# Kernel optimization log

Measured on AMD Instinct MI355X. Metric: run time of the kernel, lower is better.

The kernel has to match this reference:

```python
import jax, jax.numpy as jnp
import numpy as np

N_NODES = 50000
N_EDGES = 800000
NFEAT, NHID1, NHID2, NHID3, NCLASS = 128, 128, 128, 64, 32


def _glorot(key, fan_in, fan_out):
    lim = 1.0 / np.sqrt(fan_in)
    return jax.random.uniform(key, (fan_in, fan_out), jnp.float32, -lim, lim)


def setup_inputs() -> dict:
    key = jax.random.key(0)
    ks = jax.random.split(key, 12)
    x = jax.random.normal(ks[0], (N_NODES, NFEAT), jnp.float32)
    edge_src = jax.random.randint(ks[1], (N_EDGES,), 0, N_NODES, jnp.int32)
    edge_dst = jax.random.randint(ks[2], (N_EDGES,), 0, N_NODES, jnp.int32)
    edge_val = jax.random.uniform(ks[3], (N_EDGES,), jnp.float32)
    W1 = _glorot(ks[4], NFEAT, NHID1)
    W2 = _glorot(ks[5], NHID1, NHID2)
    W3 = _glorot(ks[6], NHID2, NHID3)
    W4 = _glorot(ks[7], NHID3, NCLASS)
    b1 = jnp.zeros((NHID1,), jnp.float32)
    b2 = jnp.zeros((NHID2,), jnp.float32)
    b3 = jnp.zeros((NHID3,), jnp.float32)
    b4 = jnp.zeros((NCLASS,), jnp.float32)
    return {"x": x, "edge_src": edge_src, "edge_dst": edge_dst, "edge_val": edge_val,
            "W1": W1, "b1": b1, "W2": W2, "b2": b2, "W3": W3, "b3": b3, "W4": W4, "b4": b4}


def _gc_layer(h, W, b, src, dst, val):
    # support = h @ W ; out = adj @ support + b  (adj in COO form)
    support = h @ W                                   # [N, d_out]
    msgs = support[src] * val[:, None]                # [E, d_out] irregular gather
    agg = jax.ops.segment_sum(msgs, dst, num_segments=N_NODES)  # scatter-add
    return agg + b


def reference(x, edge_src, edge_dst, edge_val, W1, b1, W2, b2, W3, b3, W4, b4):
    h = jax.nn.relu(_gc_layer(x, W1, b1, edge_src, edge_dst, edge_val))
    h = jax.nn.relu(_gc_layer(h, W2, b2, edge_src, edge_dst, edge_val))
    h = jax.nn.relu(_gc_layer(h, W3, b3, edge_src, edge_dst, edge_val))
    h = _gc_layer(h, W4, b4, edge_src, edge_dst, edge_val)
    return h
```

## Files before the change

kernel.cpp:

```cpp
#include <hip/hip_runtime.h>

constexpr int NNODES = 50000;
constexpr int NEDGES = 800000;
constexpr int CAP = 64;

constexpr int NPART = 8;
constexpr int PSIZE = NNODES / NPART;
constexpr int FCH = 1024;
constexpr int QCAP = 320;

constexpr int CHUNKS = (NEDGES + FCH - 1) / FCH;
constexpr int TILE_ITEMS = (NNODES + 63) / 64;
constexpr int PACK_TOT = 43008;

typedef __attribute__((ext_vector_type(8))) short short8;
typedef __attribute__((ext_vector_type(8))) unsigned short ushort8;
typedef __attribute__((ext_vector_type(4))) float f32x4;

__device__ __forceinline__ unsigned short f2b(float f) {
    unsigned int u = __float_as_uint(f);
    u += 0x7FFFu + ((u >> 16) & 1u);
    return (unsigned short)(u >> 16);
}
__device__ __forceinline__ float b2f(unsigned short u) {
    return __uint_as_float(((unsigned int)u) << 16);
}
__device__ __forceinline__ float recval(unsigned int rec) {
    return __uint_as_float(rec & 0xFFFF0000u);
}

template <int N, int K>
__device__ __forceinline__ void pack_one(int idx, const float* __restrict__ W,
                                         unsigned short* __restrict__ Wp) {
    constexpr int KS = K / 32;
    int j = idx & 7;
    int lane = (idx >> 3) & 63;
    int t = idx >> 9;
    int nt = t / KS, ks = t % KS;
    int n = nt * 16 + (lane & 15);
    int k = ks * 32 + (lane >> 4) * 8 + j;
    Wp[idx] = f2b(W[(size_t)k * N + n]);
}

__global__ __launch_bounds__(256) void prep_kernel(
        const float* __restrict__ W1, const float* __restrict__ W2,
        const float* __restrict__ W3, const float* __restrict__ W4,
        unsigned short* __restrict__ Wp1, unsigned short* __restrict__ Wp2,
        unsigned short* __restrict__ Wp3, unsigned short* __restrict__ Wp4) {
    int p = blockIdx.x * 256 + threadIdx.x;
    if (p < 16384) pack_one<128, 128>(p, W1, Wp1);
    else if (p < 32768) pack_one<128, 128>(p - 16384, W2, Wp2);
    else if (p < 40960) pack_one<64, 128>(p - 32768, W3, Wp3);
    else if (p < 43008) pack_one<32, 64>(p - 40960, W4, Wp4);
}

template <int N, int K, bool AF32>
__device__ __forceinline__ void gemm_item(int t, const void* __restrict__ Hv,
                                          const unsigned short* __restrict__ Wp,
                                          unsigned short* __restrict__ Sb) {
    constexpr int NT = N / 16, KS = K / 32;
    const int lane = threadIdx.x & 63;
    const int wave = threadIdx.x >> 6;
    const int waveRow = t * 64 + wave * 16;
    const int m = lane & 15, quad = lane >> 4;
    int arow = waveRow + m;
    if (arow >= NNODES) arow = NNODES - 1;

    f32x4 acc[NT];
#pragma unroll
    for (int nt = 0; nt < NT; ++nt) acc[nt] = (f32x4){0.f, 0.f, 0.f, 0.f};

#pragma unroll
    for (int ks = 0; ks < KS; ++ks) {
        short8 a;
        if (AF32) {
            const float* hp = (const float*)Hv + (size_t)arow * K + ks * 32 + quad * 8;
            float4 a0 = *reinterpret_cast<const float4*>(hp);
            float4 a1 = *reinterpret_cast<const float4*>(hp + 4);
            a[0] = (short)f2b(a0.x); a[1] = (short)f2b(a0.y);
            a[2] = (short)f2b(a0.z); a[3] = (short)f2b(a0.w);
            a[4] = (short)f2b(a1.x); a[5] = (short)f2b(a1.y);
            a[6] = (short)f2b(a1.z); a[7] = (short)f2b(a1.w);
        } else {
            a = *reinterpret_cast<const short8*>(
                (const unsigned short*)Hv + (size_t)arow * K + ks * 32 + quad * 8);
        }
#pragma unroll
        for (int nt = 0; nt < NT; ++nt) {
            short8 b = *reinterpret_cast<const short8*>(Wp + ((nt * KS + ks) * 64 + lane) * 8);
            acc[nt] = __builtin_amdgcn_mfma_f32_16x16x32_bf16(a, b, acc[nt], 0, 0, 0);
        }
    }

#pragma unroll
    for (int reg = 0; reg < 4; ++reg) {
        int grow = waveRow + quad * 4 + reg;
        if (grow < NNODES) {
#pragma unroll
            for (int nt = 0; nt < NT; ++nt)
                Sb[(size_t)grow * N + nt * 16 + m] = f2b(acc[nt][reg]);
        }
    }
}

__global__ __launch_bounds__(256) void fill_gemm1_kernel(
        const int* __restrict__ src, const int* __restrict__ dst,
        const float* __restrict__ val, int* __restrict__ cursor,
        unsigned int* __restrict__ buckets,
        const float* __restrict__ x, const unsigned short* __restrict__ Wp1,
        unsigned short* __restrict__ Q) {
    __shared__ unsigned int q_rec[QCAP];
    __shared__ int q_d[QCAP];
    __shared__ int qcount;

    const int g = blockIdx.x / 9;
    const int r = blockIdx.x % 9;
    if (r == 0) {
        gemm_item<128, 128, true>(g, x, Wp1, Q);
        return;
    }

    if (threadIdx.x == 0) qcount = 0;
    __syncthreads();

    const int part = blockIdx.x & 7;
    const int lo = part * PSIZE, hi = lo + PSIZE;
    const int e0 = g * FCH + threadIdx.x * 4;

    int4 d4 = make_int4(-1, -1, -1, -1);
    int4 s4 = make_int4(0, 0, 0, 0);
    float4 v4 = make_float4(0.f, 0.f, 0.f, 0.f);
    if (e0 + 3 < NEDGES) {
        d4 = *reinterpret_cast<const int4*>(dst + e0);
        s4 = *reinterpret_cast<const int4*>(src + e0);
        v4 = *reinterpret_cast<const float4*>(val + e0);
    } else if (e0 < NEDGES) {
        d4.x = dst[e0]; s4.x = src[e0]; v4.x = val[e0];
        if (e0 + 1 < NEDGES) { d4.y = dst[e0 + 1]; s4.y = src[e0 + 1]; v4.y = val[e0 + 1]; }
        if (e0 + 2 < NEDGES) { d4.z = dst[e0 + 2]; s4.z = src[e0 + 2]; v4.z = val[e0 + 2]; }
    }
    int dd[4] = {d4.x, d4.y, d4.z, d4.w};
    int ss[4] = {s4.x, s4.y, s4.z, s4.w};
    float vv[4] = {v4.x, v4.y, v4.z, v4.w};
#pragma unroll
    for (int i = 0; i < 4; ++i) {
        int d = dd[i];
        if (d >= lo && d < hi) {
            unsigned int rec = (unsigned int)ss[i] | ((unsigned int)f2b(vv[i]) << 16);
            int pos = atomicAdd(&qcount, 1);
            if (pos < QCAP) {
                q_rec[pos] = rec;
                q_d[pos] = d;
            } else {
                int p = atomicAdd(&cursor[d], 1);
                if (p < CAP) buckets[(size_t)d * CAP + p] = rec;
            }
        }
    }
    __syncthreads();

    int n = qcount < QCAP ? qcount : QCAP;
    for (int i = threadIdx.x; i < n; i += 256) {
        int d = q_d[i];
        unsigned int rec = q_rec[i];
        int p = atomicAdd(&cursor[d], 1);
        if (p < CAP) buckets[(size_t)d * CAP + p] = rec;
    }
}

template <int NIN, int NOUT>
__global__ __launch_bounds__(256) void agg_gemm_kernel(
        const unsigned short* __restrict__ Sprev, const unsigned int* __restrict__ buckets,
        const int* __restrict__ counts, const float* __restrict__ bias,
        const unsigned short* __restrict__ Wp, unsigned short* __restrict__ Snext) {
    constexpr int NCH = NIN / 8;
    constexpr int R = 256 / NCH;
    constexpr int LROW = NIN + 8;
    constexpr int KS = NIN / 32;
    constexpr int NT = NOUT / 16;
    constexpr int RT = R / 16;
    constexpr int TILES = RT * NT;
    __shared__ unsigned short htile[R * LROW];

    const int nodeBase = blockIdx.x * R;

    {
        int nl = threadIdx.x / NCH;
        int cg = threadIdx.x % NCH;
        int node = nodeBase + nl;
        float acc[8];
        if (node < NNODES) {
#pragma unroll
            for (int t = 0; t < 8; ++t) acc[t] = bias[cg * 8 + t];
            int cnt = counts[node];
            if (cnt > CAP) cnt = CAP;
            const unsigned int* eb = buckets + (size_t)node * CAP;
            int j = 0;
            for (; j + 4 <= cnt; j += 4) {
                uint4 ea = *reinterpret_cast<const uint4*>(eb + j);
                const ushort8 m0 = *reinterpret_cast<const ushort8*>(Sprev + (size_t)(ea.x & 0xFFFF) * NIN + cg * 8);
                const ushort8 m1 = *reinterpret_cast<const ushort8*>(Sprev + (size_t)(ea.y & 0xFFFF) * NIN + cg * 8);
                const ushort8 m2 = *reinterpret_cast<const ushort8*>(Sprev + (size_t)(ea.z & 0xFFFF) * NIN + cg * 8);
                const ushort8 m3 = *reinterpret_cast<const ushort8*>(Sprev + (size_t)(ea.w & 0xFFFF) * NIN + cg * 8);
                float v0 = recval(ea.x), v1 = recval(ea.y);
                float v2 = recval(ea.z), v3 = recval(ea.w);
#pragma unroll
                for (int t = 0; t < 8; ++t) {
                    acc[t] = fmaf(b2f(m0[t]), v0, acc[t]);
                    acc[t] = fmaf(b2f(m1[t]), v1, acc[t]);
                    acc[t] = fmaf(b2f(m2[t]), v2, acc[t]);
                    acc[t] = fmaf(b2f(m3[t]), v3, acc[t]);
                }
            }
            for (; j < cnt; ++j) {
                unsigned int rec = eb[j];
                float v = recval(rec);
                const ushort8 mr = *reinterpret_cast<const ushort8*>(Sprev + (size_t)(rec & 0xFFFF) * NIN + cg * 8);
#pragma unroll
                for (int t = 0; t < 8; ++t) acc[t] = fmaf(b2f(mr[t]), v, acc[t]);
            }
        } else {
#pragma unroll
            for (int t = 0; t < 8; ++t) acc[t] = 0.f;
        }
        ushort8 o;
#pragma unroll
        for (int t = 0; t < 8; ++t) o[t] = f2b(fmaxf(acc[t], 0.f));
        *reinterpret_cast<ushort8*>(&htile[nl * LROW + cg * 8]) = o;
    }
    __syncthreads();

    {
        const int lane = threadIdx.x & 63, wave = threadIdx.x >> 6;
        const int m = lane & 15, quad = lane >> 4;
        for (int t = wave; t < TILES; t += 4) {
            int rt = t / NT, nt = t % NT;
            f32x4 acc = (f32x4){0.f, 0.f, 0.f, 0.f};
#pragma unroll
            for (int ks = 0; ks < KS; ++ks) {
                short8 a = *reinterpret_cast<const short8*>(
                    &htile[(rt * 16 + m) * LROW + ks * 32 + quad * 8]);
                short8 b = *reinterpret_cast<const short8*>(Wp + ((nt * KS + ks) * 64 + lane) * 8);
                acc = __builtin_amdgcn_mfma_f32_16x16x32_bf16(a, b, acc, 0, 0, 0);
            }
#pragma unroll
            for (int reg = 0; reg < 4; ++reg) {
                int grow = nodeBase + rt * 16 + quad * 4 + reg;
                if (grow < NNODES)
                    Snext[(size_t)grow * NOUT + nt * 16 + m] = f2b(acc[reg]);
            }
        }
    }
}

__global__ __launch_bounds__(256) void agg_out_kernel(const unsigned short* __restrict__ Sb,
        const unsigned int* __restrict__ buckets, const int* __restrict__ counts,
        const float* __restrict__ bias, float* __restrict__ outp) {
    constexpr int N = 32;
    int node = blockIdx.x * 64 + threadIdx.x / 4;
    int cg = threadIdx.x % 4;
    if (node >= NNODES) return;
    int cnt = counts[node];
    if (cnt > CAP) cnt = CAP;
    const unsigned int* eb = buckets + (size_t)node * CAP;
    float acc[8];
#pragma unroll
    for (int t = 0; t < 8; ++t) acc[t] = bias[cg * 8 + t];

    int j = 0;
    for (; j + 4 <= cnt; j += 4) {
        uint4 ea = *reinterpret_cast<const uint4*>(eb + j);
        const ushort8 m0 = *reinterpret_cast<const ushort8*>(Sb + (size_t)(ea.x & 0xFFFF) * N + cg * 8);
        const ushort8 m1 = *reinterpret_cast<const ushort8*>(Sb + (size_t)(ea.y & 0xFFFF) * N + cg * 8);
        const ushort8 m2 = *reinterpret_cast<const ushort8*>(Sb + (size_t)(ea.z & 0xFFFF) * N + cg * 8);
        const ushort8 m3 = *reinterpret_cast<const ushort8*>(Sb + (size_t)(ea.w & 0xFFFF) * N + cg * 8);
        float v0 = recval(ea.x), v1 = recval(ea.y);
        float v2 = recval(ea.z), v3 = recval(ea.w);
#pragma unroll
        for (int t = 0; t < 8; ++t) {
            acc[t] = fmaf(b2f(m0[t]), v0, acc[t]);
            acc[t] = fmaf(b2f(m1[t]), v1, acc[t]);
            acc[t] = fmaf(b2f(m2[t]), v2, acc[t]);
            acc[t] = fmaf(b2f(m3[t]), v3, acc[t]);
        }
    }
    for (; j < cnt; ++j) {
        unsigned int rec = eb[j];
        float v = recval(rec);
        const ushort8 mr = *reinterpret_cast<const ushort8*>(Sb + (size_t)(rec & 0xFFFF) * N + cg * 8);
#pragma unroll
        for (int t = 0; t < 8; ++t) acc[t] = fmaf(b2f(mr[t]), v, acc[t]);
    }

    float* op = outp + (size_t)node * N + cg * 8;
    *reinterpret_cast<float4*>(op) = make_float4(acc[0], acc[1], acc[2], acc[3]);
    *reinterpret_cast<float4*>(op + 4) = make_float4(acc[4], acc[5], acc[6], acc[7]);
}

extern "C" void kernel_launch(void* const* d_in, const int* in_sizes, int n_in,
                              void* d_out, int out_size, void* d_ws, size_t ws_size,
                              hipStream_t stream) {
    const float* x   = (const float*)d_in[0];
    const int*   src = (const int*)d_in[1];
    const int*   dst = (const int*)d_in[2];
    const float* val = (const float*)d_in[3];
    const float* W1  = (const float*)d_in[4];
    const float* b1  = (const float*)d_in[5];
    const float* W2  = (const float*)d_in[6];
    const float* b2  = (const float*)d_in[7];
    const float* W3  = (const float*)d_in[8];
    const float* b3  = (const float*)d_in[9];
    const float* W4  = (const float*)d_in[10];
    const float* b4  = (const float*)d_in[11];
    float* out = (float*)d_out;

    unsigned short* P = (unsigned short*)d_ws;
    unsigned short* Q = P + (size_t)NNODES * 128;
    unsigned int* buckets = (unsigned int*)(Q + (size_t)NNODES * 128);
    unsigned short* Wp1 = (unsigned short*)(buckets + (size_t)NNODES * CAP);
    unsigned short* Wp2 = Wp1 + 128 * 128;
    unsigned short* Wp3 = Wp2 + 128 * 128;
    unsigned short* Wp4 = Wp3 + 128 * 64;
    int* cursor = (int*)(Wp4 + 64 * 32);

    const dim3 blk(256);

    hipMemsetAsync(cursor, 0, NNODES * sizeof(int), stream);
    prep_kernel<<<(PACK_TOT + 255) / 256, blk, 0, stream>>>(W1, W2, W3, W4,
                                                            Wp1, Wp2, Wp3, Wp4);
    fill_gemm1_kernel<<<CHUNKS * 9, blk, 0, stream>>>(
        src, dst, val, cursor, buckets, x, Wp1, Q);
    agg_gemm_kernel<128, 128><<<(NNODES + 15) / 16, blk, 0, stream>>>(
        Q, buckets, cursor, b1, Wp2, P);
    agg_gemm_kernel<128, 64><<<(NNODES + 15) / 16, blk, 0, stream>>>(
        P, buckets, cursor, b2, Wp3, Q);
    agg_gemm_kernel<64, 32><<<(NNODES + 31) / 32, blk, 0, stream>>>(
        Q, buckets, cursor, b3, Wp4, P);
    agg_out_kernel<<<(NNODES + 63) / 64, blk, 0, stream>>>(P, buckets, cursor, b4, out);
}
```

Measured before the change: 220.6 us.

## Replace fixed-capacity edge buckets with compact CSR built by histogram and scan

The fixed 64-slot per-node bucket array is replaced by a compact CSR layout. A degree histogram is fused with the first GEMM, followed by a two-pass prefix scan (rows padded to multiples of 4) and a scatter pass that writes edge records into contiguous rows. This shrinks the edge storage footprint and makes aggregation reads contiguous. It also removes the CAP truncation, so high-degree nodes are no longer silently dropped. The aggregation loop is unrolled to 8 edges to keep more gathers in flight, at the cost of two extra scan launches and a separate histogram pass over dst.

```diff
diff --git a/kernel.cpp b/kernel.cpp
--- a/kernel.cpp
+++ b/kernel.cpp
@@ -2,15 +2,16 @@
 
 constexpr int NNODES = 50000;
 constexpr int NEDGES = 800000;
-constexpr int CAP = 64;
 
 constexpr int NPART = 8;
 constexpr int PSIZE = NNODES / NPART;
 constexpr int FCH = 1024;
 constexpr int QCAP = 320;
-
 constexpr int CHUNKS = (NEDGES + FCH - 1) / FCH;
 constexpr int TILE_ITEMS = (NNODES + 63) / 64;
+constexpr int HCH = 512;
+constexpr int SCAN_BLOCKS = (NNODES + 255) / 256;
+constexpr int RECCAP = NEDGES + 3 * NNODES + 272;
 constexpr int PACK_TOT = 43008;
 
 typedef __attribute__((ext_vector_type(8))) short short8;
@@ -103,29 +104,81 @@
     }
 }
 
-__global__ __launch_bounds__(256) void fill_gemm1_kernel(
+__global__ __launch_bounds__(256) void gemm1_hist_kernel(
+        const float* __restrict__ x, const unsigned short* __restrict__ Wp1,
+        unsigned short* __restrict__ Q,
+        const int* __restrict__ dst, int* __restrict__ deg) {
+    const int g = blockIdx.x / 3;
+    const int r = blockIdx.x % 3;
+    if (r == 0) {
+        gemm_item<128, 128, true>(g, x, Wp1, Q);
+        return;
+    }
+    const int c = g * 2 + (r - 1);
+    const int e0 = c * HCH + threadIdx.x * 2;
+    if (e0 + 1 < NEDGES) {
+        int2 d2 = *reinterpret_cast<const int2*>(dst + e0);
+        atomicAdd(&deg[d2.x], 1);
+        atomicAdd(&deg[d2.y], 1);
+    } else if (e0 < NEDGES) {
+        atomicAdd(&deg[dst[e0]], 1);
+    }
+}
+
+__global__ __launch_bounds__(256) void scan1_kernel(const int* __restrict__ deg,
+        int* __restrict__ rowstart, int* __restrict__ blockSums) {
+    __shared__ int s[256];
+    const int b = blockIdx.x, tid = threadIdx.x;
+    const int i = b * 256 + tid;
+    int c = 0;
+    if (i < NNODES) c = (deg[i] + 3) & ~3;
+    s[tid] = c;
+    __syncthreads();
+    for (int o = 1; o < 256; o <<= 1) {
+        int t = (tid >= o) ? s[tid - o] : 0;
+        __syncthreads();
+        s[tid] += t;
+        __syncthreads();
+    }
+    if (i < NNODES) rowstart[i] = s[tid] - c;
+    if (tid == 255) blockSums[b] = s[255];
+}
+
+__global__ __launch_bounds__(256) void scan2_kernel(const int* __restrict__ blockSums,
+        int* __restrict__ rowstart, int* __restrict__ cursor) {
+    __shared__ int s[256];
+    const int b = blockIdx.x, tid = threadIdx.x;
+    s[tid] = (tid < SCAN_BLOCKS) ? blockSums[tid] : 0;
+    __syncthreads();
+    for (int o = 1; o < 256; o <<= 1) {
+        int t = (tid >= o) ? s[tid - o] : 0;
+        __syncthreads();
+        s[tid] += t;
+        __syncthreads();
+    }
+    const int off = (b == 0) ? 0 : s[b - 1];
+    const int i = b * 256 + tid;
+    if (i < NNODES) {
+        int rs = rowstart[i] + off;
+        rowstart[i] = rs;
+        cursor[i] = rs;
+    }
+}
+
+__global__ __launch_bounds__(256) void scatter_kernel(
         const int* __restrict__ src, const int* __restrict__ dst,
         const float* __restrict__ val, int* __restrict__ cursor,
-        unsigned int* __restrict__ buckets,
-        const float* __restrict__ x, const unsigned short* __restrict__ Wp1,
-        unsigned short* __restrict__ Q) {
+        unsigned int* __restrict__ rec) {
     __shared__ unsigned int q_rec[QCAP];
     __shared__ int q_d[QCAP];
     __shared__ int qcount;
-
-    const int g = blockIdx.x / 9;
-    const int r = blockIdx.x % 9;
-    if (r == 0) {
-        gemm_item<128, 128, true>(g, x, Wp1, Q);
-        return;
-    }
-
     if (threadIdx.x == 0) qcount = 0;
     __syncthreads();
 
     const int part = blockIdx.x & 7;
+    const int chunk = blockIdx.x >> 3;
     const int lo = part * PSIZE, hi = lo + PSIZE;
-    const int e0 = g * FCH + threadIdx.x * 4;
+    const int e0 = chunk * FCH + threadIdx.x * 4;
 
     int4 d4 = make_int4(-1, -1, -1, -1);
     int4 s4 = make_int4(0, 0, 0, 0);
@@ -146,14 +199,14 @@
     for (int i = 0; i < 4; ++i) {
         int d = dd[i];
         if (d >= lo && d < hi) {
-            unsigned int rec = (unsigned int)ss[i] | ((unsigned int)f2b(vv[i]) << 16);
+            unsigned int r = (unsigned int)ss[i] | ((unsigned int)f2b(vv[i]) << 16);
             int pos = atomicAdd(&qcount, 1);
             if (pos < QCAP) {
-                q_rec[pos] = rec;
+                q_rec[pos] = r;
                 q_d[pos] = d;
             } else {
                 int p = atomicAdd(&cursor[d], 1);
-                if (p < CAP) buckets[(size_t)d * CAP + p] = rec;
+                rec[p] = r;
             }
         }
     }
@@ -162,16 +215,72 @@
     int n = qcount < QCAP ? qcount : QCAP;
     for (int i = threadIdx.x; i < n; i += 256) {
         int d = q_d[i];
-        unsigned int rec = q_rec[i];
         int p = atomicAdd(&cursor[d], 1);
-        if (p < CAP) buckets[(size_t)d * CAP + p] = rec;
+        rec[p] = q_rec[i];
+    }
+}
+
+template <int NIN>
+__device__ __forceinline__ void pull_agg(const unsigned short* __restrict__ Sprev,
+                                         const unsigned int* __restrict__ eb,
+                                         int cnt, int cg, float* __restrict__ acc) {
+    const unsigned short* Sp = Sprev + cg * 8;
+    int j = 0;
+    for (; j + 8 <= cnt; j += 8) {
+        uint4 ea = *reinterpret_cast<const uint4*>(eb + j);
+        uint4 ec = *reinterpret_cast<const uint4*>(eb + j + 4);
+        const ushort8 m0 = *reinterpret_cast<const ushort8*>(Sp + (ea.x & 0xFFFFu) * (unsigned)NIN);
+        const ushort8 m1 = *reinterpret_cast<const ushort8*>(Sp + (ea.y & 0xFFFFu) * (unsigned)NIN);
+        const ushort8 m2 = *reinterpret_cast<const ushort8*>(Sp + (ea.z & 0xFFFFu) * (unsigned)NIN);
+        const ushort8 m3 = *reinterpret_cast<const ushort8*>(Sp + (ea.w & 0xFFFFu) * (unsigned)NIN);
+        const ushort8 m4 = *reinterpret_cast<const ushort8*>(Sp + (ec.x & 0xFFFFu) * (unsigned)NIN);
+        const ushort8 m5 = *reinterpret_cast<const ushort8*>(Sp + (ec.y & 0xFFFFu) * (unsigned)NIN);
+        const ushort8 m6 = *reinterpret_cast<const ushort8*>(Sp + (ec.z & 0xFFFFu) * (unsigned)NIN);
+        const ushort8 m7 = *reinterpret_cast<const ushort8*>(Sp + (ec.w & 0xFFFFu) * (unsigned)NIN);
+        float v0 = recval(ea.x), v1 = recval(ea.y), v2 = recval(ea.z), v3 = recval(ea.w);
+        float v4 = recval(ec.x), v5 = recval(ec.y), v6 = recval(ec.z), v7 = recval(ec.w);
+#pragma unroll
+        for (int t = 0; t < 8; ++t) {
+            acc[t] = fmaf(b2f(m0[t]), v0, acc[t]);
+            acc[t] = fmaf(b2f(m1[t]), v1, acc[t]);
+            acc[t] = fmaf(b2f(m2[t]), v2, acc[t]);
+            acc[t] = fmaf(b2f(m3[t]), v3, acc[t]);
+            acc[t] = fmaf(b2f(m4[t]), v4, acc[t]);
+            acc[t] = fmaf(b2f(m5[t]), v5, acc[t]);
+            acc[t] = fmaf(b2f(m6[t]), v6, acc[t]);
+            acc[t] = fmaf(b2f(m7[t]), v7, acc[t]);
+        }
+    }
+    for (; j + 4 <= cnt; j += 4) {
+        uint4 ea = *reinterpret_cast<const uint4*>(eb + j);
+        const ushort8 m0 = *reinterpret_cast<const ushort8*>(Sp + (ea.x & 0xFFFFu) * (unsigned)NIN);
+        const ushort8 m1 = *reinterpret_cast<const ushort8*>(Sp + (ea.y & 0xFFFFu) * (unsigned)NIN);
+        const ushort8 m2 = *reinterpret_cast<const ushort8*>(Sp + (ea.z & 0xFFFFu) * (unsigned)NIN);
+        const ushort8 m3 = *reinterpret_cast<const ushort8*>(Sp + (ea.w & 0xFFFFu) * (unsigned)NIN);
+        float v0 = recval(ea.x), v1 = recval(ea.y);
+        float v2 = recval(ea.z), v3 = recval(ea.w);
+#pragma unroll
+        for (int t = 0; t < 8; ++t) {
+            acc[t] = fmaf(b2f(m0[t]), v0, acc[t]);
+            acc[t] = fmaf(b2f(m1[t]), v1, acc[t]);
+            acc[t] = fmaf(b2f(m2[t]), v2, acc[t]);
+            acc[t] = fmaf(b2f(m3[t]), v3, acc[t]);
+        }
+    }
+    for (; j < cnt; ++j) {
+        unsigned int r = eb[j];
+        float v = recval(r);
+        const ushort8 mr = *reinterpret_cast<const ushort8*>(Sp + (r & 0xFFFFu) * (unsigned)NIN);
+#pragma unroll
+        for (int t = 0; t < 8; ++t) acc[t] = fmaf(b2f(mr[t]), v, acc[t]);
     }
 }
 
 template <int NIN, int NOUT>
 __global__ __launch_bounds__(256) void agg_gemm_kernel(
-        const unsigned short* __restrict__ Sprev, const unsigned int* __restrict__ buckets,
-        const int* __restrict__ counts, const float* __restrict__ bias,
+        const unsigned short* __restrict__ Sprev, const unsigned int* __restrict__ rec,
+        const int* __restrict__ rowstart, const int* __restrict__ rowend,
+        const float* __restrict__ bias,
         const unsigned short* __restrict__ Wp, unsigned short* __restrict__ Snext) {
     constexpr int NCH = NIN / 8;
     constexpr int R = 256 / NCH;
@@ -192,33 +301,9 @@
         if (node < NNODES) {
 #pragma unroll
             for (int t = 0; t < 8; ++t) acc[t] = bias[cg * 8 + t];
-            int cnt = counts[node];
-            if (cnt > CAP) cnt = CAP;
-            const unsigned int* eb = buckets + (size_t)node * CAP;
-            int j = 0;
-            for (; j + 4 <= cnt; j += 4) {
-                uint4 ea = *reinterpret_cast<const uint4*>(eb + j);
-                const ushort8 m0 = *reinterpret_cast<const ushort8*>(Sprev + (size_t)(ea.x & 0xFFFF) * NIN + cg * 8);
-                const ushort8 m1 = *reinterpret_cast<const ushort8*>(Sprev + (size_t)(ea.y & 0xFFFF) * NIN + cg * 8);
-                const ushort8 m2 = *reinterpret_cast<const ushort8*>(Sprev + (size_t)(ea.z & 0xFFFF) * NIN + cg * 8);
-                const ushort8 m3 = *reinterpret_cast<const ushort8*>(Sprev + (size_t)(ea.w & 0xFFFF) * NIN + cg * 8);
-                float v0 = recval(ea.x), v1 = recval(ea.y);
-                float v2 = recval(ea.z), v3 = recval(ea.w);
-#pragma unroll
-                for (int t = 0; t < 8; ++t) {
-                    acc[t] = fmaf(b2f(m0[t]), v0, acc[t]);
-                    acc[t] = fmaf(b2f(m1[t]), v1, acc[t]);
-                    acc[t] = fmaf(b2f(m2[t]), v2, acc[t]);
-                    acc[t] = fmaf(b2f(m3[t]), v3, acc[t]);
-                }
-            }
-            for (; j < cnt; ++j) {
-                unsigned int rec = eb[j];
-                float v = recval(rec);
-                const ushort8 mr = *reinterpret_cast<const ushort8*>(Sprev + (size_t)(rec & 0xFFFF) * NIN + cg * 8);
-#pragma unroll
-                for (int t = 0; t < 8; ++t) acc[t] = fmaf(b2f(mr[t]), v, acc[t]);
-            }
+            int start = rowstart[node];
+            int cnt = rowend[node] - start;
+            pull_agg<NIN>(Sprev, rec + start, cnt, cg, acc);
         } else {
 #pragma unroll
             for (int t = 0; t < 8; ++t) acc[t] = 0.f;
@@ -254,43 +339,20 @@
 }
 
 __global__ __launch_bounds__(256) void agg_out_kernel(const unsigned short* __restrict__ Sb,
-        const unsigned int* __restrict__ buckets, const int* __restrict__ counts,
-        const float* __restrict__ bias, float* __restrict__ outp) {
+        const unsigned int* __restrict__ rec, const int* __restrict__ rowstart,
+        const int* __restrict__ rowend, const float* __restrict__ bias,
+        float* __restrict__ outp) {
     constexpr int N = 32;
     int node = blockIdx.x * 64 + threadIdx.x / 4;
     int cg = threadIdx.x % 4;
     if (node >= NNODES) return;
-    int cnt = counts[node];
-    if (cnt > CAP) cnt = CAP;
-    const unsigned int* eb = buckets + (size_t)node * CAP;
     float acc[8];
 #pragma unroll
     for (int t = 0; t < 8; ++t) acc[t] = bias[cg * 8 + t];
 
-    int j = 0;
-    for (; j + 4 <= cnt; j += 4) {
-        uint4 ea = *reinterpret_cast<const uint4*>(eb + j);
-        const ushort8 m0 = *reinterpret_cast<const ushort8*>(Sb + (size_t)(ea.x & 0xFFFF) * N + cg * 8);
-        const ushort8 m1 = *reinterpret_cast<const ushort8*>(Sb + (size_t)(ea.y & 0xFFFF) * N + cg * 8);
-        const ushort8 m2 = *reinterpret_cast<const ushort8*>(Sb + (size_t)(ea.z & 0xFFFF) * N + cg * 8);
-        const ushort8 m3 = *reinterpret_cast<const ushort8*>(Sb + (size_t)(ea.w & 0xFFFF) * N + cg * 8);
-        float v0 = recval(ea.x), v1 = recval(ea.y);
-        float v2 = recval(ea.z), v3 = recval(ea.w);
-#pragma unroll
-        for (int t = 0; t < 8; ++t) {
-            acc[t] = fmaf(b2f(m0[t]), v0, acc[t]);
-            acc[t] = fmaf(b2f(m1[t]), v1, acc[t]);
-            acc[t] = fmaf(b2f(m2[t]), v2, acc[t]);
-            acc[t] = fmaf(b2f(m3[t]), v3, acc[t]);
-        }
-    }
-    for (; j < cnt; ++j) {
-        unsigned int rec = eb[j];
-        float v = recval(rec);
-        const ushort8 mr = *reinterpret_cast<const ushort8*>(Sb + (size_t)(rec & 0xFFFF) * N + cg * 8);
-#pragma unroll
-        for (int t = 0; t < 8; ++t) acc[t] = fmaf(b2f(mr[t]), v, acc[t]);
-    }
+    int start = rowstart[node];
+    int cnt = rowend[node] - start;
+    pull_agg<N>(Sb, rec + start, cnt, cg, acc);
 
     float* op = outp + (size_t)node * N + cg * 8;
     *reinterpret_cast<float4*>(op) = make_float4(acc[0], acc[1], acc[2], acc[3]);
@@ -316,25 +378,30 @@
 
     unsigned short* P = (unsigned short*)d_ws;
     unsigned short* Q = P + (size_t)NNODES * 128;
-    unsigned int* buckets = (unsigned int*)(Q + (size_t)NNODES * 128);
-    unsigned short* Wp1 = (unsigned short*)(buckets + (size_t)NNODES * CAP);
+    unsigned int* rec = (unsigned int*)(Q + (size_t)NNODES * 128);
+    int* deg       = (int*)(rec + RECCAP);
+    int* rowstart  = deg + NNODES;
+    int* cursor    = rowstart + NNODES;
+    int* blockSums = cursor + NNODES;
+    unsigned short* Wp1 = (unsigned short*)(blockSums + 256);
     unsigned short* Wp2 = Wp1 + 128 * 128;
     unsigned short* Wp3 = Wp2 + 128 * 128;
     unsigned short* Wp4 = Wp3 + 128 * 64;
-    int* cursor = (int*)(Wp4 + 64 * 32);
 
     const dim3 blk(256);
 
-    hipMemsetAsync(cursor, 0, NNODES * sizeof(int), stream);
+    hipMemsetAsync(deg, 0, NNODES * sizeof(int), stream);
     prep_kernel<<<(PACK_TOT + 255) / 256, blk, 0, stream>>>(W1, W2, W3, W4,
                                                             Wp1, Wp2, Wp3, Wp4);
-    fill_gemm1_kernel<<<CHUNKS * 9, blk, 0, stream>>>(
-        src, dst, val, cursor, buckets, x, Wp1, Q);
+    gemm1_hist_kernel<<<TILE_ITEMS * 3, blk, 0, stream>>>(x, Wp1, Q, dst, deg);
+    scan1_kernel<<<SCAN_BLOCKS, blk, 0, stream>>>(deg, rowstart, blockSums);
+    scan2_kernel<<<SCAN_BLOCKS, blk, 0, stream>>>(blockSums, rowstart, cursor);
+    scatter_kernel<<<CHUNKS * 8, blk, 0, stream>>>(src, dst, val, cursor, rec);
     agg_gemm_kernel<128, 128><<<(NNODES + 15) / 16, blk, 0, stream>>>(
-        Q, buckets, cursor, b1, Wp2, P);
+        Q, rec, rowstart, cursor, b1, Wp2, P);
     agg_gemm_kernel<128, 64><<<(NNODES + 15) / 16, blk, 0, stream>>>(
-        P, buckets, cursor, b2, Wp3, Q);
+        P, rec, rowstart, cursor, b2, Wp3, Q);
     agg_gemm_kernel<64, 32><<<(NNODES + 31) / 32, blk, 0, stream>>>(
-        Q, buckets, cursor, b3, Wp4, P);
-    agg_out_kernel<<<(NNODES + 63) / 64, blk, 0, stream>>>(P, buckets, cursor, b4, out);
-}
+        Q, rec, rowstart, cursor, b3, Wp4, P);
+    agg_out_kernel<<<(NNODES + 63) / 64, blk, 0, stream>>>(P, rec, rowstart, cursor, b4, out);
+}
```

New measurement: 261.3 us. 18.5% more time.

## Replace 8-pass edge bucketing with single-pass partition plus scatter kernel

Applied to the files above, without the earlier changes.

Previously the fill kernel ran 8 blocks per edge chunk, each rereading the chunk and keeping only edges whose destination fell in one node partition. Now each edge chunk is read once: edges are staged in shared memory per partition, flushed as 64-bit (dst, record) entries into per-partition global segments, and a separate scatter kernel then does the per-node cursor atomics into buckets. The cursor memset is folded into the weight-pack kernel, and the shared gather-accumulate loop is unrolled to 8 edges. This trades the redundant edge reads for an extra kernel launch and an extra write and read of an 8-byte-per-edge intermediate buffer. The scatter grid interleaves partitions across consecutive blocks, which may weaken the cache locality of the cursor atomics.

```diff
diff --git a/kernel.cpp b/kernel.cpp
--- a/kernel.cpp
+++ b/kernel.cpp
@@ -7,10 +7,11 @@
 constexpr int NPART = 8;
 constexpr int PSIZE = NNODES / NPART;
 constexpr int FCH = 1024;
-constexpr int QCAP = 320;
-
 constexpr int CHUNKS = (NEDGES + FCH - 1) / FCH;
 constexpr int TILE_ITEMS = (NNODES + 63) / 64;
+constexpr int LCAP = 192;
+constexpr int SEGSTRIDE = 131072;
+constexpr int SCHUNKS = SEGSTRIDE / FCH;
 constexpr int PACK_TOT = 43008;
 
 typedef __attribute__((ext_vector_type(8))) short short8;
@@ -46,8 +47,11 @@
         const float* __restrict__ W1, const float* __restrict__ W2,
         const float* __restrict__ W3, const float* __restrict__ W4,
         unsigned short* __restrict__ Wp1, unsigned short* __restrict__ Wp2,
-        unsigned short* __restrict__ Wp3, unsigned short* __restrict__ Wp4) {
+        unsigned short* __restrict__ Wp3, unsigned short* __restrict__ Wp4,
+        int* __restrict__ cursor, int* __restrict__ pcur) {
     int p = blockIdx.x * 256 + threadIdx.x;
+    if (p < NNODES) cursor[p] = 0;
+    if (p < 8) pcur[p] = 0;
     if (p < 16384) pack_one<128, 128>(p, W1, Wp1);
     else if (p < 32768) pack_one<128, 128>(p - 16384, W2, Wp2);
     else if (p < 40960) pack_one<64, 128>(p - 32768, W3, Wp3);
@@ -103,31 +107,27 @@
     }
 }
 
-__global__ __launch_bounds__(256) void fill_gemm1_kernel(
+__global__ __launch_bounds__(256) void gemm1_part_kernel(
+        const float* __restrict__ x, const unsigned short* __restrict__ Wp1,
+        unsigned short* __restrict__ Q,
         const int* __restrict__ src, const int* __restrict__ dst,
-        const float* __restrict__ val, int* __restrict__ cursor,
-        unsigned int* __restrict__ buckets,
-        const float* __restrict__ x, const unsigned short* __restrict__ Wp1,
-        unsigned short* __restrict__ Q) {
-    __shared__ unsigned int q_rec[QCAP];
-    __shared__ int q_d[QCAP];
-    __shared__ int qcount;
-
-    const int g = blockIdx.x / 9;
-    const int r = blockIdx.x % 9;
-    if (r == 0) {
+        const float* __restrict__ val,
+        int* __restrict__ pcur, unsigned long long* __restrict__ seg) {
+    __shared__ unsigned long long ls[8][LCAP];
+    __shared__ int lcnt[8];
+    __shared__ int gbase[8];
+
+    const int g = blockIdx.x >> 1;
+    if (blockIdx.x & 1) {
         gemm_item<128, 128, true>(g, x, Wp1, Q);
         return;
     }
 
-    if (threadIdx.x == 0) qcount = 0;
+    if (threadIdx.x < 8) lcnt[threadIdx.x] = 0;
     __syncthreads();
 
-    const int part = blockIdx.x & 7;
-    const int lo = part * PSIZE, hi = lo + PSIZE;
     const int e0 = g * FCH + threadIdx.x * 4;
-
-    int4 d4 = make_int4(-1, -1, -1, -1);
+    int4 d4 = make_int4(0, 0, 0, 0);
     int4 s4 = make_int4(0, 0, 0, 0);
     float4 v4 = make_float4(0.f, 0.f, 0.f, 0.f);
     if (e0 + 3 < NEDGES) {
@@ -144,27 +144,128 @@
     float vv[4] = {v4.x, v4.y, v4.z, v4.w};
 #pragma unroll
     for (int i = 0; i < 4; ++i) {
-        int d = dd[i];
-        if (d >= lo && d < hi) {
-            unsigned int rec = (unsigned int)ss[i] | ((unsigned int)f2b(vv[i]) << 16);
-            int pos = atomicAdd(&qcount, 1);
-            if (pos < QCAP) {
-                q_rec[pos] = rec;
-                q_d[pos] = d;
-            } else {
-                int p = atomicAdd(&cursor[d], 1);
-                if (p < CAP) buckets[(size_t)d * CAP + p] = rec;
+        if (e0 + i < NEDGES) {
+            int d = dd[i];
+            int part = d / PSIZE;
+            unsigned long long r = (unsigned long long)(unsigned)d |
+                ((unsigned long long)((unsigned)ss[i] | ((unsigned)f2b(vv[i]) << 16)) << 32);
+            int pos = atomicAdd(&lcnt[part], 1);
+            if (pos < LCAP) ls[part][pos] = r;
+            else {
+                int p = atomicAdd(&pcur[part], 1);
+                if (p < SEGSTRIDE) seg[(size_t)part * SEGSTRIDE + p] = r;
             }
         }
     }
     __syncthreads();
 
-    int n = qcount < QCAP ? qcount : QCAP;
-    for (int i = threadIdx.x; i < n; i += 256) {
-        int d = q_d[i];
-        unsigned int rec = q_rec[i];
-        int p = atomicAdd(&cursor[d], 1);
-        if (p < CAP) buckets[(size_t)d * CAP + p] = rec;
+    if (threadIdx.x < 8) {
+        int c = lcnt[threadIdx.x]; if (c > LCAP) c = LCAP;
+        gbase[threadIdx.x] = atomicAdd(&pcur[threadIdx.x], c);
+    }
+    __syncthreads();
+
+    int pre[9]; pre[0] = 0;
+#pragma unroll
+    for (int t = 0; t < 8; ++t) {
+        int c = lcnt[t]; if (c > LCAP) c = LCAP;
+        pre[t + 1] = pre[t] + c;
+    }
+    const int total = pre[8];
+    for (int i = threadIdx.x; i < total; i += 256) {
+        int part = 0;
+#pragma unroll
+        for (int t = 1; t < 8; ++t) part += (i >= pre[t]);
+        int off = i - pre[part];
+        int p = gbase[part] + off;
+        if (p < SEGSTRIDE) seg[(size_t)part * SEGSTRIDE + p] = ls[part][off];
+    }
+}
+
+__global__ __launch_bounds__(256) void scatter_kernel(
+        const unsigned long long* __restrict__ seg, const int* __restrict__ pcur,
+        int* __restrict__ cursor, unsigned int* __restrict__ buckets) {
+    const int part = blockIdx.x & 7;
+    const int chunk = blockIdx.x >> 3;
+    int cnt = pcur[part]; if (cnt > SEGSTRIDE) cnt = SEGSTRIDE;
+    const int r0 = chunk * FCH + threadIdx.x * 4;
+    if (r0 >= cnt) return;
+    const unsigned long long* sp = seg + (size_t)part * SEGSTRIDE;
+    if (r0 + 3 < cnt) {
+        uint4 a = *reinterpret_cast<const uint4*>(sp + r0);
+        uint4 b = *reinterpret_cast<const uint4*>(sp + r0 + 2);
+        int p0 = atomicAdd(&cursor[(int)a.x], 1);
+        if (p0 < CAP) buckets[(size_t)(int)a.x * CAP + p0] = a.y;
+        int p1 = atomicAdd(&cursor[(int)a.z], 1);
+        if (p1 < CAP) buckets[(size_t)(int)a.z * CAP + p1] = a.w;
+        int p2 = atomicAdd(&cursor[(int)b.x], 1);
+        if (p2 < CAP) buckets[(size_t)(int)b.x * CAP + p2] = b.y;
+        int p3 = atomicAdd(&cursor[(int)b.z], 1);
+        if (p3 < CAP) buckets[(size_t)(int)b.z * CAP + p3] = b.w;
+    } else {
+        for (int i = 0; i < cnt - r0; ++i) {
+            unsigned long long r = sp[r0 + i];
+            int d = (int)(unsigned)(r & 0xFFFFFFFFull);
+            unsigned int rc = (unsigned int)(r >> 32);
+            int p = atomicAdd(&cursor[d], 1);
+            if (p < CAP) buckets[(size_t)d * CAP + p] = rc;
+        }
+    }
+}
+
+template <int NIN>
+__device__ __forceinline__ void pull_agg(const unsigned short* __restrict__ Sprev,
+                                         const unsigned int* __restrict__ eb,
+                                         int cnt, int cg, float* __restrict__ acc) {
+    const unsigned short* Sp = Sprev + cg * 8;
+    int j = 0;
+    for (; j + 8 <= cnt; j += 8) {
+        uint4 ea = *reinterpret_cast<const uint4*>(eb + j);
+        uint4 ec = *reinterpret_cast<const uint4*>(eb + j + 4);
+        const ushort8 m0 = *reinterpret_cast<const ushort8*>(Sp + (ea.x & 0xFFFFu) * (unsigned)NIN);
+        const ushort8 m1 = *reinterpret_cast<const ushort8*>(Sp + (ea.y & 0xFFFFu) * (unsigned)NIN);
+        const ushort8 m2 = *reinterpret_cast<const ushort8*>(Sp + (ea.z & 0xFFFFu) * (unsigned)NIN);
+        const ushort8 m3 = *reinterpret_cast<const ushort8*>(Sp + (ea.w & 0xFFFFu) * (unsigned)NIN);
+        const ushort8 m4 = *reinterpret_cast<const ushort8*>(Sp + (ec.x & 0xFFFFu) * (unsigned)NIN);
+        const ushort8 m5 = *reinterpret_cast<const ushort8*>(Sp + (ec.y & 0xFFFFu) * (unsigned)NIN);
+        const ushort8 m6 = *reinterpret_cast<const ushort8*>(Sp + (ec.z & 0xFFFFu) * (unsigned)NIN);
+        const ushort8 m7 = *reinterpret_cast<const ushort8*>(Sp + (ec.w & 0xFFFFu) * (unsigned)NIN);
+        float v0 = recval(ea.x), v1 = recval(ea.y), v2 = recval(ea.z), v3 = recval(ea.w);
+        float v4 = recval(ec.x), v5 = recval(ec.y), v6 = recval(ec.z), v7 = recval(ec.w);
+#pragma unroll
+        for (int t = 0; t < 8; ++t) {
+            acc[t] = fmaf(b2f(m0[t]), v0, acc[t]);
+            acc[t] = fmaf(b2f(m1[t]), v1, acc[t]);
+            acc[t] = fmaf(b2f(m2[t]), v2, acc[t]);
+            acc[t] = fmaf(b2f(m3[t]), v3, acc[t]);
+            acc[t] = fmaf(b2f(m4[t]), v4, acc[t]);
+            acc[t] = fmaf(b2f(m5[t]), v5, acc[t]);
+            acc[t] = fmaf(b2f(m6[t]), v6, acc[t]);
+            acc[t] = fmaf(b2f(m7[t]), v7, acc[t]);
+        }
+    }
+    for (; j + 4 <= cnt; j += 4) {
+        uint4 ea = *reinterpret_cast<const uint4*>(eb + j);
+        const ushort8 m0 = *reinterpret_cast<const ushort8*>(Sp + (ea.x & 0xFFFFu) * (unsigned)NIN);
+        const ushort8 m1 = *reinterpret_cast<const ushort8*>(Sp + (ea.y & 0xFFFFu) * (unsigned)NIN);
+        const ushort8 m2 = *reinterpret_cast<const ushort8*>(Sp + (ea.z & 0xFFFFu) * (unsigned)NIN);
+        const ushort8 m3 = *reinterpret_cast<const ushort8*>(Sp + (ea.w & 0xFFFFu) * (unsigned)NIN);
+        float v0 = recval(ea.x), v1 = recval(ea.y);
+        float v2 = recval(ea.z), v3 = recval(ea.w);
+#pragma unroll
+        for (int t = 0; t < 8; ++t) {
+            acc[t] = fmaf(b2f(m0[t]), v0, acc[t]);
+            acc[t] = fmaf(b2f(m1[t]), v1, acc[t]);
+            acc[t] = fmaf(b2f(m2[t]), v2, acc[t]);
+            acc[t] = fmaf(b2f(m3[t]), v3, acc[t]);
+        }
+    }
+    for (; j < cnt; ++j) {
+        unsigned int r = eb[j];
+        float v = recval(r);
+        const ushort8 mr = *reinterpret_cast<const ushort8*>(Sp + (r & 0xFFFFu) * (unsigned)NIN);
+#pragma unroll
+        for (int t = 0; t < 8; ++t) acc[t] = fmaf(b2f(mr[t]), v, acc[t]);
     }
 }
 
@@ -194,31 +295,7 @@
             for (int t = 0; t < 8; ++t) acc[t] = bias[cg * 8 + t];
             int cnt = counts[node];
             if (cnt > CAP) cnt = CAP;
-            const unsigned int* eb = buckets + (size_t)node * CAP;
-            int j = 0;
-            for (; j + 4 <= cnt; j += 4) {
-                uint4 ea = *reinterpret_cast<const uint4*>(eb + j);
-                const ushort8 m0 = *reinterpret_cast<const ushort8*>(Sprev + (size_t)(ea.x & 0xFFFF) * NIN + cg * 8);
-                const ushort8 m1 = *reinterpret_cast<const ushort8*>(Sprev + (size_t)(ea.y & 0xFFFF) * NIN + cg * 8);
-                const ushort8 m2 = *reinterpret_cast<const ushort8*>(Sprev + (size_t)(ea.z & 0xFFFF) * NIN + cg * 8);
-                const ushort8 m3 = *reinterpret_cast<const ushort8*>(Sprev + (size_t)(ea.w & 0xFFFF) * NIN + cg * 8);
-                float v0 = recval(ea.x), v1 = recval(ea.y);
-                float v2 = recval(ea.z), v3 = recval(ea.w);
-#pragma unroll
-                for (int t = 0; t < 8; ++t) {
-                    acc[t] = fmaf(b2f(m0[t]), v0, acc[t]);
-                    acc[t] = fmaf(b2f(m1[t]), v1, acc[t]);
-                    acc[t] = fmaf(b2f(m2[t]), v2, acc[t]);
-                    acc[t] = fmaf(b2f(m3[t]), v3, acc[t]);
-                }
-            }
-            for (; j < cnt; ++j) {
-                unsigned int rec = eb[j];
-                float v = recval(rec);
-                const ushort8 mr = *reinterpret_cast<const ushort8*>(Sprev + (size_t)(rec & 0xFFFF) * NIN + cg * 8);
-#pragma unroll
-                for (int t = 0; t < 8; ++t) acc[t] = fmaf(b2f(mr[t]), v, acc[t]);
-            }
+            pull_agg<NIN>(Sprev, buckets + (size_t)node * CAP, cnt, cg, acc);
         } else {
 #pragma unroll
             for (int t = 0; t < 8; ++t) acc[t] = 0.f;
@@ -260,37 +337,13 @@
     int node = blockIdx.x * 64 + threadIdx.x / 4;
     int cg = threadIdx.x % 4;
     if (node >= NNODES) return;
+    float acc[8];
+#pragma unroll
+    for (int t = 0; t < 8; ++t) acc[t] = bias[cg * 8 + t];
+
     int cnt = counts[node];
     if (cnt > CAP) cnt = CAP;
-    const unsigned int* eb = buckets + (size_t)node * CAP;
-    float acc[8];
-#pragma unroll
-    for (int t = 0; t < 8; ++t) acc[t] = bias[cg * 8 + t];
-
-    int j = 0;
-    for (; j + 4 <= cnt; j += 4) {
-        uint4 ea = *reinterpret_cast<const uint4*>(eb + j);
-        const ushort8 m0 = *reinterpret_cast<const ushort8*>(Sb + (size_t)(ea.x & 0xFFFF) * N + cg * 8);
-        const ushort8 m1 = *reinterpret_cast<const ushort8*>(Sb + (size_t)(ea.y & 0xFFFF) * N + cg * 8);
-        const ushort8 m2 = *reinterpret_cast<const ushort8*>(Sb + (size_t)(ea.z & 0xFFFF) * N + cg * 8);
-        const ushort8 m3 = *reinterpret_cast<const ushort8*>(Sb + (size_t)(ea.w & 0xFFFF) * N + cg * 8);
-        float v0 = recval(ea.x), v1 = recval(ea.y);
-        float v2 = recval(ea.z), v3 = recval(ea.w);
-#pragma unroll
-        for (int t = 0; t < 8; ++t) {
-            acc[t] = fmaf(b2f(m0[t]), v0, acc[t]);
-            acc[t] = fmaf(b2f(m1[t]), v1, acc[t]);
-            acc[t] = fmaf(b2f(m2[t]), v2, acc[t]);
-            acc[t] = fmaf(b2f(m3[t]), v3, acc[t]);
-        }
-    }
-    for (; j < cnt; ++j) {
-        unsigned int rec = eb[j];
-        float v = recval(rec);
-        const ushort8 mr = *reinterpret_cast<const ushort8*>(Sb + (size_t)(rec & 0xFFFF) * N + cg * 8);
-#pragma unroll
-        for (int t = 0; t < 8; ++t) acc[t] = fmaf(b2f(mr[t]), v, acc[t]);
-    }
+    pull_agg<N>(Sb, buckets + (size_t)node * CAP, cnt, cg, acc);
 
     float* op = outp + (size_t)node * N + cg * 8;
     *reinterpret_cast<float4*>(op) = make_float4(acc[0], acc[1], acc[2], acc[3]);
@@ -317,19 +370,21 @@
     unsigned short* P = (unsigned short*)d_ws;
     unsigned short* Q = P + (size_t)NNODES * 128;
     unsigned int* buckets = (unsigned int*)(Q + (size_t)NNODES * 128);
-    unsigned short* Wp1 = (unsigned short*)(buckets + (size_t)NNODES * CAP);
+    unsigned long long* seg = (unsigned long long*)(buckets + (size_t)NNODES * CAP);
+    int* cursor = (int*)(seg + (size_t)NPART * SEGSTRIDE);
+    int* pcur = cursor + NNODES;
+    unsigned short* Wp1 = (unsigned short*)(pcur + 8);
     unsigned short* Wp2 = Wp1 + 128 * 128;
     unsigned short* Wp3 = Wp2 + 128 * 128;
     unsigned short* Wp4 = Wp3 + 128 * 64;
-    int* cursor = (int*)(Wp4 + 64 * 32);
 
     const dim3 blk(256);
 
-    hipMemsetAsync(cursor, 0, NNODES * sizeof(int), stream);
-    prep_kernel<<<(PACK_TOT + 255) / 256, blk, 0, stream>>>(W1, W2, W3, W4,
-                                                            Wp1, Wp2, Wp3, Wp4);
-    fill_gemm1_kernel<<<CHUNKS * 9, blk, 0, stream>>>(
-        src, dst, val, cursor, buckets, x, Wp1, Q);
+    prep_kernel<<<(NNODES + 255) / 256, blk, 0, stream>>>(
+        W1, W2, W3, W4, Wp1, Wp2, Wp3, Wp4, cursor, pcur);
+    gemm1_part_kernel<<<TILE_ITEMS * 2, blk, 0, stream>>>(
+        x, Wp1, Q, src, dst, val, pcur, seg);
+    scatter_kernel<<<NPART * SCHUNKS, blk, 0, stream>>>(seg, pcur, cursor, buckets);
     agg_gemm_kernel<128, 128><<<(NNODES + 15) / 16, blk, 0, stream>>>(
         Q, buckets, cursor, b1, Wp2, P);
     agg_gemm_kernel<128, 64><<<(NNODES + 15) / 16, blk, 0, stream>>>(
```

After: 235.3 us. +6.7%, slower.
